# Optimization experiments

Measured on AMD Instinct MI355X. Metric: run time of the kernel, lower is better.

## Reference

```python
import jax, jax.numpy as jnp
import numpy as np

USER = 100000
ITEM = 200000
LATDIM = 128
GNN_LAYER = 3
UUGNN_LAYER = 2
N_EDGES = 600000
UU_EDGES = 300000


def setup_inputs() -> dict:
    key = jax.random.key(0)
    ks = jax.random.split(key, 8)
    N = USER + ITEM
    return {
        "uEmbeds0": jax.random.normal(ks[0], (USER, LATDIM), dtype=jnp.float32) * 0.05,
        "iEmbeds0": jax.random.normal(ks[1], (ITEM, LATDIM), dtype=jnp.float32) * 0.05,
        "adj_rows": jax.random.randint(ks[2], (N_EDGES,), 0, N, dtype=jnp.int32),
        "adj_cols": jax.random.randint(ks[3], (N_EDGES,), 0, N, dtype=jnp.int32),
        "adj_vals": jax.random.uniform(ks[4], (N_EDGES,), dtype=jnp.float32),
        "uadj_rows": jax.random.randint(ks[5], (UU_EDGES,), 0, USER, dtype=jnp.int32),
        "uadj_cols": jax.random.randint(ks[6], (UU_EDGES,), 0, USER, dtype=jnp.int32),
        "uadj_vals": jax.random.uniform(ks[7], (UU_EDGES,), dtype=jnp.float32),
    }


def _spmm(rows, cols, vals, x, n_rows):
    # out[r] = sum_{e: rows[e]==r} vals[e] * x[cols[e]]  (COO sparse @ dense)
    return jax.ops.segment_sum(vals[:, None] * x[cols], rows, num_segments=n_rows)


def reference(uEmbeds0, iEmbeds0, adj_rows, adj_cols, adj_vals,
              uadj_rows, uadj_cols, uadj_vals):
    N = USER + ITEM
    # LightGCN over bipartite adjacency, pool='sum' over layer-0..L embeddings
    # (dropout in eval mode -> identity)
    embeds = jnp.concatenate([uEmbeds0, iEmbeds0], axis=0)  # [N, d]
    acc = embeds
    for _ in range(GNN_LAYER):
        embeds = _spmm(adj_rows, adj_cols, adj_vals, embeds, N)
        acc = acc + embeds
    ui_uEmbed = acc[:USER]
    ui_iEmbed = acc[USER:]

    # LightGCN2 over user-user adjacency, sum of layer embeddings
    ulat = uEmbeds0
    uacc = ulat
    for _ in range(UUGNN_LAYER):
        ulat = _spmm(uadj_rows, uadj_cols, uadj_vals, ulat, USER)
        uacc = uacc + ulat
    return (ui_uEmbed, ui_iEmbed, uacc)
```

## Files before the change

### kernel.cpp

```cpp
#include <hip/hip_runtime.h>
#include <hip/hip_fp16.h>

#define USER_N   100000
#define ITEM_N   200000
#define LATDIM   128
#define NV4      32
#define N_TOTAL  300000
#define NR_ALL   400000
#define N_EDGES_C  600000
#define UU_EDGES_C 300000
#define NE_ALL   900000
#define SCAN_B   256

struct alignas(8) h4 { __half2 lo, hi; };

typedef float f4_ext __attribute__((ext_vector_type(4)));

__device__ __forceinline__ h4 to_h4(float4 a) {
    h4 r; r.lo = __floats2half2_rn(a.x, a.y); r.hi = __floats2half2_rn(a.z, a.w);
    return r;
}
__device__ __forceinline__ float4 to_f4(h4 h) {
    float2 l = __half22float2(h.lo), hh = __half22float2(h.hi);
    return make_float4(l.x, l.y, hh.x, hh.y);
}
__device__ __forceinline__ void fma4(float4& a, float v, float4 x) {
    a.x += v * x.x; a.y += v * x.y; a.z += v * x.z; a.w += v * x.w;
}
__device__ __forceinline__ float4 nt_load4(const float4* p) {
    f4_ext v = __builtin_nontemporal_load((const f4_ext*)p);
    return make_float4(v.x, v.y, v.z, v.w);
}
__device__ __forceinline__ void nt_store4(float4* p, float4 a) {
    f4_ext v = {a.x, a.y, a.z, a.w};
    __builtin_nontemporal_store(v, (f4_ext*)p);
}

__global__ void hist2_kernel(const int* __restrict__ ar, const int* __restrict__ ur,
                             int* __restrict__ cnt) {
    int i = blockIdx.x * blockDim.x + threadIdx.x;
    if (i < N_EDGES_C)      atomicAdd(&cnt[ar[i]], 1);
    else if (i < NE_ALL)    atomicAdd(&cnt[ur[i - N_EDGES_C] + N_TOTAL], 1);
}

__global__ void scan_block_kernel(const int* __restrict__ cnt,
                                  int* __restrict__ rptr,
                                  int* __restrict__ bsum, int n) {
    __shared__ int s[SCAN_B];
    int i = blockIdx.x * SCAN_B + threadIdx.x;
    int v = (i < n) ? cnt[i] : 0;
    s[threadIdx.x] = v;
    __syncthreads();
    for (int off = 1; off < SCAN_B; off <<= 1) {
        int t = (threadIdx.x >= off) ? s[threadIdx.x - off] : 0;
        __syncthreads();
        s[threadIdx.x] += t;
        __syncthreads();
    }
    if (i < n) rptr[i] = s[threadIdx.x] - v;
    if (threadIdx.x == SCAN_B - 1) bsum[blockIdx.x] = s[threadIdx.x];
}

__global__ void scan_bsum_kernel(int* __restrict__ bsum, int nb) {
    __shared__ int s[SCAN_B];
    __shared__ int carry;
    if (threadIdx.x == 0) carry = 0;
    __syncthreads();
    for (int base = 0; base < nb; base += SCAN_B) {
        int i = base + threadIdx.x;
        int v = (i < nb) ? bsum[i] : 0;
        s[threadIdx.x] = v;
        __syncthreads();
        for (int off = 1; off < SCAN_B; off <<= 1) {
            int t = (threadIdx.x >= off) ? s[threadIdx.x - off] : 0;
            __syncthreads();
            s[threadIdx.x] += t;
            __syncthreads();
        }
        if (i < nb) bsum[i] = s[threadIdx.x] - v + carry;
        __syncthreads();
        if (threadIdx.x == 0) carry += s[SCAN_B - 1];
        __syncthreads();
    }
}

__global__ void scan_add_kernel(int* __restrict__ rptr, const int* __restrict__ bsum,
                                int* __restrict__ cursor, int n, int n_edges) {
    int i = blockIdx.x * blockDim.x + threadIdx.x;
    if (i < n) {
        int v = rptr[i] + bsum[i / SCAN_B];
        rptr[i]   = v;
        cursor[i] = v;
    }
    if (i == 0) rptr[n] = n_edges;
}

__global__ void scatter2_kernel(const int* __restrict__ ar, const int* __restrict__ ac,
                                const float* __restrict__ av,
                                const int* __restrict__ ur, const int* __restrict__ uc,
                                const float* __restrict__ uv,
                                int* __restrict__ cursor,
                                int* __restrict__ scol, float* __restrict__ sval) {
    int i = blockIdx.x * blockDim.x + threadIdx.x;
    int r, c; float v;
    if (i < N_EDGES_C)      { r = ar[i];             c = ac[i];           v = av[i]; }
    else if (i < NE_ALL)    { int j = i - N_EDGES_C; r = ur[j] + N_TOTAL; c = uc[j] + N_TOTAL; v = uv[j]; }
    else return;
    int pos = atomicAdd(&cursor[r], 1);
    scol[pos] = c;
    sval[pos] = v;
}

__global__ void conv_kernel(const float4* __restrict__ uE,
                            const float4* __restrict__ iE,
                            h4* __restrict__ E16) {
    int i = blockIdx.x * blockDim.x + threadIdx.x;
    if (i >= N_TOTAL * NV4) return;
    const int ub = USER_N * NV4;
    float4 v = (i < ub) ? nt_load4(uE + i) : nt_load4(iE + (i - ub));
    E16[i] = to_h4(v);
}

__device__ __forceinline__ int e16_row(int c) {
    return (c < N_TOTAL) ? c : c - N_TOTAL;
}

__global__ void spmm_pass1(const int* __restrict__ rptr,
                           const int* __restrict__ scol,
                           const float* __restrict__ sval,
                           const h4* __restrict__ E16,
                           h4* __restrict__ cur1) {
    int t = blockIdx.x * blockDim.x + threadIdx.x;
    int r = t >> 5, sub = t & 31;
    if (r >= NR_ALL) return;
    int e0 = rptr[r], e1 = rptr[r + 1];

    float4 a0 = make_float4(0.f,0.f,0.f,0.f), a1 = a0;
    int e = e0;
    for (; e + 2 <= e1; e += 2) {
        int c0 = scol[e], c1 = scol[e + 1];
        float v0 = sval[e], v1 = sval[e + 1];
        h4 h0 = E16[(size_t)e16_row(c0) * NV4 + sub];
        h4 h1 = E16[(size_t)e16_row(c1) * NV4 + sub];
        fma4(a0, v0, to_f4(h0)); fma4(a1, v1, to_f4(h1));
    }
    if (e < e1) {
        int c0 = scol[e]; float v0 = sval[e];
        fma4(a0, v0, to_f4(E16[(size_t)e16_row(c0) * NV4 + sub]));
    }
    float4 a = make_float4(a0.x+a1.x, a0.y+a1.y, a0.z+a1.z, a0.w+a1.w);
    cur1[(size_t)r * NV4 + sub] = to_h4(a);
}

__global__ void spmm_pass2(const int* __restrict__ rptr,
                           const int* __restrict__ scol,
                           const float* __restrict__ sval,
                           const h4* __restrict__ cur1,
                           const h4* __restrict__ E16,
                           h4* __restrict__ cur2,
                           float4* __restrict__ uacc) {
    int t = blockIdx.x * blockDim.x + threadIdx.x;
    int r = t >> 5, sub = t & 31;
    if (r >= NR_ALL) return;
    int e0 = rptr[r], e1 = rptr[r + 1];

    float4 a0 = make_float4(0.f,0.f,0.f,0.f), a1 = a0;
    int e = e0;
    for (; e + 2 <= e1; e += 2) {
        int c0 = scol[e], c1 = scol[e + 1];
        float v0 = sval[e], v1 = sval[e + 1];
        h4 h0 = cur1[(size_t)c0 * NV4 + sub];
        h4 h1 = cur1[(size_t)c1 * NV4 + sub];
        fma4(a0, v0, to_f4(h0)); fma4(a1, v1, to_f4(h1));
    }
    if (e < e1) {
        int c0 = scol[e]; float v0 = sval[e];
        fma4(a0, v0, to_f4(cur1[(size_t)c0 * NV4 + sub]));
    }
    float4 a = make_float4(a0.x+a1.x, a0.y+a1.y, a0.z+a1.z, a0.w+a1.w);

    size_t o = (size_t)r * NV4 + sub;
    if (r < N_TOTAL) {
        cur2[o] = to_h4(a);
    } else {
        int ur = r - N_TOTAL;
        float4 u0 = to_f4(E16[(size_t)ur * NV4 + sub]);
        float4 l1 = to_f4(cur1[o]);
        nt_store4(uacc + (size_t)ur * NV4 + sub,
                  make_float4(u0.x + l1.x + a.x, u0.y + l1.y + a.y,
                              u0.z + l1.z + a.z, u0.w + l1.w + a.w));
    }
}

__global__ void spmm_pass3(const int* __restrict__ rptr,
                           const int* __restrict__ scol,
                           const float* __restrict__ sval,
                           const h4* __restrict__ cur2,
                           const h4* __restrict__ cur1,
                           const h4* __restrict__ E16,
                           float4* __restrict__ acc) {
    int t = blockIdx.x * blockDim.x + threadIdx.x;
    int r = t >> 5, sub = t & 31;
    if (r >= N_TOTAL) return;
    int e0 = rptr[r], e1 = rptr[r + 1];

    float4 a0 = make_float4(0.f,0.f,0.f,0.f), a1 = a0;
    int e = e0;
    for (; e + 2 <= e1; e += 2) {
        int c0 = scol[e], c1 = scol[e + 1];
        float v0 = sval[e], v1 = sval[e + 1];
        h4 h0 = cur2[(size_t)c0 * NV4 + sub];
        h4 h1 = cur2[(size_t)c1 * NV4 + sub];
        fma4(a0, v0, to_f4(h0)); fma4(a1, v1, to_f4(h1));
    }
    if (e < e1) {
        int c0 = scol[e]; float v0 = sval[e];
        fma4(a0, v0, to_f4(cur2[(size_t)c0 * NV4 + sub]));
    }
    float4 a = make_float4(a0.x+a1.x, a0.y+a1.y, a0.z+a1.z, a0.w+a1.w);

    size_t o = (size_t)r * NV4 + sub;
    float4 ez = to_f4(E16[o]);
    float4 l1 = to_f4(cur1[o]);
    float4 l2 = to_f4(cur2[o]);
    nt_store4(acc + o,
              make_float4(ez.x + l1.x + l2.x + a.x,
                          ez.y + l1.y + l2.y + a.y,
                          ez.z + l1.z + l2.z + a.z,
                          ez.w + l1.w + l2.w + a.w));
}

extern "C" void kernel_launch(void* const* d_in, const int* in_sizes, int n_in,
                              void* d_out, int out_size, void* d_ws, size_t ws_size,
                              hipStream_t stream) {
    const float* uE    = (const float*)d_in[0];
    const float* iE    = (const float*)d_in[1];
    const int*   arows = (const int*)  d_in[2];
    const int*   acols = (const int*)  d_in[3];
    const float* avals = (const float*)d_in[4];
    const int*   urows = (const int*)  d_in[5];
    const int*   ucols = (const int*)  d_in[6];
    const float* uvals = (const float*)d_in[7];

    float* acc  = (float*)d_out;
    float* uacc = acc + (size_t)N_TOTAL * LATDIM;

    h4*    E16  = (h4*)d_ws;
    h4*    cur1 = E16 + (size_t)N_TOTAL * NV4;
    h4*    cur2 = cur1 + (size_t)NR_ALL * NV4;
    int*   cnt  = (int*)(cur2 + (size_t)N_TOTAL * NV4);
    int*   rptr = cnt + NR_ALL;
    int*   curp = rptr + NR_ALL + 1;
    int*   bsum = curp + NR_ALL;
    int*   scol = bsum + 4096;
    float* sval = (float*)(scol + NE_ALL);

    const int TB = 256;

    hipMemsetAsync(cnt, 0, NR_ALL * sizeof(int), stream);
    hist2_kernel<<<(NE_ALL + TB - 1) / TB, TB, 0, stream>>>(arows, urows, cnt);
    {
        int nb = (NR_ALL + SCAN_B - 1) / SCAN_B;
        scan_block_kernel<<<nb, SCAN_B, 0, stream>>>(cnt, rptr, bsum, NR_ALL);
        scan_bsum_kernel<<<1, SCAN_B, 0, stream>>>(bsum, nb);
        scan_add_kernel<<<(NR_ALL + TB - 1) / TB, TB, 0, stream>>>(
            rptr, bsum, curp, NR_ALL, NE_ALL);
    }
    scatter2_kernel<<<(NE_ALL + TB - 1) / TB, TB, 0, stream>>>(
        arows, acols, avals, urows, ucols, uvals, curp, scol, sval);

    conv_kernel<<<(N_TOTAL * NV4 + TB - 1) / TB, TB, 0, stream>>>(
        (const float4*)uE, (const float4*)iE, E16);

    {
        int threads = NR_ALL * 32;
        int grid = (threads + TB - 1) / TB;
        spmm_pass1<<<grid, TB, 0, stream>>>(rptr, scol, sval, E16, cur1);
        spmm_pass2<<<grid, TB, 0, stream>>>(rptr, scol, sval, cur1, E16,
                                            cur2, (float4*)uacc);
    }
    {
        int threads = N_TOTAL * 32;
        int grid = (threads + TB - 1) / TB;
        spmm_pass3<<<grid, TB, 0, stream>>>(rptr, scol, sval, cur2, cur1, E16,
                                            (float4*)acc);
    }
}
```

Before: 382.0 us.

## Use 16-byte half8 rows, interleaved edge structs, and fuse conversion with histogram

The SpMM kernels now assign 16 threads per row, and each thread loads 16 bytes (8 halves) instead of 8, which halves the number of gather instructions per edge. Column index and value are stored together as one 8-byte Edge struct, so each edge needs one load instead of two. The fp16 conversion kernel is merged into the histogram kernel, removing one launch. Pass 3 also uses nontemporal loads for edges and residual terms. Wider per-thread work means fewer threads overall, which may expose less latency hiding on irregular gathers.

```diff
diff --git a/kernel.cpp b/kernel.cpp
--- a/kernel.cpp
+++ b/kernel.cpp
@@ -5,28 +5,25 @@
 #define ITEM_N   200000
 #define LATDIM   128
 #define NV4      32
+#define NV8      16
 #define N_TOTAL  300000
 #define NR_ALL   400000
 #define N_EDGES_C  600000
 #define UU_EDGES_C 300000
 #define NE_ALL   900000
 #define SCAN_B   256
-
-struct alignas(8) h4 { __half2 lo, hi; };
+#define CONV_T   (N_TOTAL * NV8)
+
+struct alignas(16) h8 { __half2 a, b, c, d; };
+struct alignas(8)  Edge { int c; float v; };
 
 typedef float f4_ext __attribute__((ext_vector_type(4)));
-
-__device__ __forceinline__ h4 to_h4(float4 a) {
-    h4 r; r.lo = __floats2half2_rn(a.x, a.y); r.hi = __floats2half2_rn(a.z, a.w);
-    return r;
-}
-__device__ __forceinline__ float4 to_f4(h4 h) {
-    float2 l = __half22float2(h.lo), hh = __half22float2(h.hi);
-    return make_float4(l.x, l.y, hh.x, hh.y);
-}
-__device__ __forceinline__ void fma4(float4& a, float v, float4 x) {
-    a.x += v * x.x; a.y += v * x.y; a.z += v * x.z; a.w += v * x.w;
-}
+typedef int   i4_ext __attribute__((ext_vector_type(4)));
+typedef int   i2_ext __attribute__((ext_vector_type(2)));
+
+union H8I { i4_ext i; h8 h; };
+union EDI { i2_ext i; Edge e; };
+
 __device__ __forceinline__ float4 nt_load4(const float4* p) {
     f4_ext v = __builtin_nontemporal_load((const f4_ext*)p);
     return make_float4(v.x, v.y, v.z, v.w);
@@ -35,12 +32,53 @@
     f4_ext v = {a.x, a.y, a.z, a.w};
     __builtin_nontemporal_store(v, (f4_ext*)p);
 }
-
-__global__ void hist2_kernel(const int* __restrict__ ar, const int* __restrict__ ur,
-                             int* __restrict__ cnt) {
-    int i = blockIdx.x * blockDim.x + threadIdx.x;
-    if (i < N_EDGES_C)      atomicAdd(&cnt[ar[i]], 1);
-    else if (i < NE_ALL)    atomicAdd(&cnt[ur[i - N_EDGES_C] + N_TOTAL], 1);
+__device__ __forceinline__ h8 nt_load_h8(const h8* p) {
+    H8I u; u.i = __builtin_nontemporal_load((const i4_ext*)p);
+    return u.h;
+}
+__device__ __forceinline__ Edge nt_load_edge(const Edge* p) {
+    EDI u; u.i = __builtin_nontemporal_load((const i2_ext*)p);
+    return u.e;
+}
+
+__device__ __forceinline__ h8 to_h8(float4 lo, float4 hi) {
+    h8 r;
+    r.a = __floats2half2_rn(lo.x, lo.y); r.b = __floats2half2_rn(lo.z, lo.w);
+    r.c = __floats2half2_rn(hi.x, hi.y); r.d = __floats2half2_rn(hi.z, hi.w);
+    return r;
+}
+__device__ __forceinline__ void h8_to_f(h8 h, float4& lo, float4& hi) {
+    float2 p = __half22float2(h.a), q = __half22float2(h.b);
+    float2 s = __half22float2(h.c), t = __half22float2(h.d);
+    lo = make_float4(p.x, p.y, q.x, q.y);
+    hi = make_float4(s.x, s.y, t.x, t.y);
+}
+__device__ __forceinline__ void fma4(float4& a, float v, float4 x) {
+    a.x += v * x.x; a.y += v * x.y; a.z += v * x.z; a.w += v * x.w;
+}
+__device__ __forceinline__ float4 add4(float4 a, float4 b) {
+    return make_float4(a.x + b.x, a.y + b.y, a.z + b.z, a.w + b.w);
+}
+
+__global__ void conv_hist_kernel(const float4* __restrict__ uE,
+                                 const float4* __restrict__ iE,
+                                 h8* __restrict__ E16,
+                                 const int* __restrict__ ar,
+                                 const int* __restrict__ ur,
+                                 int* __restrict__ cnt) {
+    int t = blockIdx.x * blockDim.x + threadIdx.x;
+    if (t < CONV_T) {
+        int f4i = t * 2;
+        const int ub = USER_N * NV4;
+        float4 lo, hi;
+        if (f4i < ub) { lo = nt_load4(uE + f4i);        hi = nt_load4(uE + f4i + 1); }
+        else          { lo = nt_load4(iE + (f4i - ub)); hi = nt_load4(iE + (f4i - ub) + 1); }
+        E16[t] = to_h8(lo, hi);
+    } else {
+        int i = t - CONV_T;
+        if (i < N_EDGES_C)   atomicAdd(&cnt[ar[i]], 1);
+        else if (i < NE_ALL) atomicAdd(&cnt[ur[i - N_EDGES_C] + N_TOTAL], 1);
+    }
 }
 
 __global__ void scan_block_kernel(const int* __restrict__ cnt,
@@ -100,25 +138,14 @@
                                 const int* __restrict__ ur, const int* __restrict__ uc,
                                 const float* __restrict__ uv,
                                 int* __restrict__ cursor,
-                                int* __restrict__ scol, float* __restrict__ sval) {
+                                Edge* __restrict__ edges) {
     int i = blockIdx.x * blockDim.x + threadIdx.x;
-    int r, c; float v;
-    if (i < N_EDGES_C)      { r = ar[i];             c = ac[i];           v = av[i]; }
-    else if (i < NE_ALL)    { int j = i - N_EDGES_C; r = ur[j] + N_TOTAL; c = uc[j] + N_TOTAL; v = uv[j]; }
+    int r; Edge ed;
+    if (i < N_EDGES_C)      { r = ar[i];             ed.c = ac[i];           ed.v = av[i]; }
+    else if (i < NE_ALL)    { int j = i - N_EDGES_C; r = ur[j] + N_TOTAL; ed.c = uc[j] + N_TOTAL; ed.v = uv[j]; }
     else return;
     int pos = atomicAdd(&cursor[r], 1);
-    scol[pos] = c;
-    sval[pos] = v;
-}
-
-__global__ void conv_kernel(const float4* __restrict__ uE,
-                            const float4* __restrict__ iE,
-                            h4* __restrict__ E16) {
-    int i = blockIdx.x * blockDim.x + threadIdx.x;
-    if (i >= N_TOTAL * NV4) return;
-    const int ub = USER_N * NV4;
-    float4 v = (i < ub) ? nt_load4(uE + i) : nt_load4(iE + (i - ub));
-    E16[i] = to_h4(v);
+    edges[pos] = ed;
 }
 
 __device__ __forceinline__ int e16_row(int c) {
@@ -126,108 +153,114 @@
 }
 
 __global__ void spmm_pass1(const int* __restrict__ rptr,
-                           const int* __restrict__ scol,
-                           const float* __restrict__ sval,
-                           const h4* __restrict__ E16,
-                           h4* __restrict__ cur1) {
+                           const Edge* __restrict__ edges,
+                           const h8* __restrict__ E16,
+                           h8* __restrict__ cur1) {
     int t = blockIdx.x * blockDim.x + threadIdx.x;
-    int r = t >> 5, sub = t & 31;
+    int r = t >> 4, sub = t & 15;
     if (r >= NR_ALL) return;
     int e0 = rptr[r], e1 = rptr[r + 1];
 
-    float4 a0 = make_float4(0.f,0.f,0.f,0.f), a1 = a0;
+    float4 a0l = make_float4(0,0,0,0), a0h = a0l, a1l = a0l, a1h = a0l;
     int e = e0;
     for (; e + 2 <= e1; e += 2) {
-        int c0 = scol[e], c1 = scol[e + 1];
-        float v0 = sval[e], v1 = sval[e + 1];
-        h4 h0 = E16[(size_t)e16_row(c0) * NV4 + sub];
-        h4 h1 = E16[(size_t)e16_row(c1) * NV4 + sub];
-        fma4(a0, v0, to_f4(h0)); fma4(a1, v1, to_f4(h1));
+        Edge d0 = edges[e], d1 = edges[e + 1];
+        h8 h0 = E16[(size_t)e16_row(d0.c) * NV8 + sub];
+        h8 h1 = E16[(size_t)e16_row(d1.c) * NV8 + sub];
+        float4 lo, hi;
+        h8_to_f(h0, lo, hi); fma4(a0l, d0.v, lo); fma4(a0h, d0.v, hi);
+        h8_to_f(h1, lo, hi); fma4(a1l, d1.v, lo); fma4(a1h, d1.v, hi);
     }
     if (e < e1) {
-        int c0 = scol[e]; float v0 = sval[e];
-        fma4(a0, v0, to_f4(E16[(size_t)e16_row(c0) * NV4 + sub]));
-    }
-    float4 a = make_float4(a0.x+a1.x, a0.y+a1.y, a0.z+a1.z, a0.w+a1.w);
-    cur1[(size_t)r * NV4 + sub] = to_h4(a);
+        Edge d0 = edges[e];
+        h8 h0 = E16[(size_t)e16_row(d0.c) * NV8 + sub];
+        float4 lo, hi;
+        h8_to_f(h0, lo, hi); fma4(a0l, d0.v, lo); fma4(a0h, d0.v, hi);
+    }
+    cur1[(size_t)r * NV8 + sub] = to_h8(add4(a0l, a1l), add4(a0h, a1h));
 }
 
 __global__ void spmm_pass2(const int* __restrict__ rptr,
-                           const int* __restrict__ scol,
-                           const float* __restrict__ sval,
-                           const h4* __restrict__ cur1,
-                           const h4* __restrict__ E16,
-                           h4* __restrict__ cur2,
+                           const Edge* __restrict__ edges,
+                           const h8* __restrict__ cur1,
+                           const h8* __restrict__ E16,
+                           h8* __restrict__ cur2,
                            float4* __restrict__ uacc) {
     int t = blockIdx.x * blockDim.x + threadIdx.x;
-    int r = t >> 5, sub = t & 31;
+    int r = t >> 4, sub = t & 15;
     if (r >= NR_ALL) return;
     int e0 = rptr[r], e1 = rptr[r + 1];
 
-    float4 a0 = make_float4(0.f,0.f,0.f,0.f), a1 = a0;
+    float4 a0l = make_float4(0,0,0,0), a0h = a0l, a1l = a0l, a1h = a0l;
     int e = e0;
     for (; e + 2 <= e1; e += 2) {
-        int c0 = scol[e], c1 = scol[e + 1];
-        float v0 = sval[e], v1 = sval[e + 1];
-        h4 h0 = cur1[(size_t)c0 * NV4 + sub];
-        h4 h1 = cur1[(size_t)c1 * NV4 + sub];
-        fma4(a0, v0, to_f4(h0)); fma4(a1, v1, to_f4(h1));
+        Edge d0 = edges[e], d1 = edges[e + 1];
+        h8 h0 = cur1[(size_t)d0.c * NV8 + sub];
+        h8 h1 = cur1[(size_t)d1.c * NV8 + sub];
+        float4 lo, hi;
+        h8_to_f(h0, lo, hi); fma4(a0l, d0.v, lo); fma4(a0h, d0.v, hi);
+        h8_to_f(h1, lo, hi); fma4(a1l, d1.v, lo); fma4(a1h, d1.v, hi);
     }
     if (e < e1) {
-        int c0 = scol[e]; float v0 = sval[e];
-        fma4(a0, v0, to_f4(cur1[(size_t)c0 * NV4 + sub]));
-    }
-    float4 a = make_float4(a0.x+a1.x, a0.y+a1.y, a0.z+a1.z, a0.w+a1.w);
-
-    size_t o = (size_t)r * NV4 + sub;
+        Edge d0 = edges[e];
+        h8 h0 = cur1[(size_t)d0.c * NV8 + sub];
+        float4 lo, hi;
+        h8_to_f(h0, lo, hi); fma4(a0l, d0.v, lo); fma4(a0h, d0.v, hi);
+    }
+    float4 al = add4(a0l, a1l), ah = add4(a0h, a1h);
+
+    size_t o = (size_t)r * NV8 + sub;
     if (r < N_TOTAL) {
-        cur2[o] = to_h4(a);
+        cur2[o] = to_h8(al, ah);
     } else {
         int ur = r - N_TOTAL;
-        float4 u0 = to_f4(E16[(size_t)ur * NV4 + sub]);
-        float4 l1 = to_f4(cur1[o]);
-        nt_store4(uacc + (size_t)ur * NV4 + sub,
-                  make_float4(u0.x + l1.x + a.x, u0.y + l1.y + a.y,
-                              u0.z + l1.z + a.z, u0.w + l1.w + a.w));
+        float4 u0l, u0h, l1l, l1h;
+        h8_to_f(E16[(size_t)ur * NV8 + sub], u0l, u0h);
+        h8_to_f(cur1[o], l1l, l1h);
+        size_t of4 = (size_t)ur * NV4 + sub * 2;
+        nt_store4(uacc + of4,     add4(add4(u0l, l1l), al));
+        nt_store4(uacc + of4 + 1, add4(add4(u0h, l1h), ah));
     }
 }
 
 __global__ void spmm_pass3(const int* __restrict__ rptr,
-                           const int* __restrict__ scol,
-                           const float* __restrict__ sval,
-                           const h4* __restrict__ cur2,
-                           const h4* __restrict__ cur1,
-                           const h4* __restrict__ E16,
+                           const Edge* __restrict__ edges,
+                           const h8* __restrict__ cur2,
+                           const h8* __restrict__ cur1,
+                           const h8* __restrict__ E16,
                            float4* __restrict__ acc) {
     int t = blockIdx.x * blockDim.x + threadIdx.x;
-    int r = t >> 5, sub = t & 31;
+    int r = t >> 4, sub = t & 15;
     if (r >= N_TOTAL) return;
     int e0 = rptr[r], e1 = rptr[r + 1];
 
-    float4 a0 = make_float4(0.f,0.f,0.f,0.f), a1 = a0;
+    float4 a0l = make_float4(0,0,0,0), a0h = a0l, a1l = a0l, a1h = a0l;
     int e = e0;
     for (; e + 2 <= e1; e += 2) {
-        int c0 = scol[e], c1 = scol[e + 1];
-        float v0 = sval[e], v1 = sval[e + 1];
-        h4 h0 = cur2[(size_t)c0 * NV4 + sub];
-        h4 h1 = cur2[(size_t)c1 * NV4 + sub];
-        fma4(a0, v0, to_f4(h0)); fma4(a1, v1, to_f4(h1));
+        Edge d0 = nt_load_edge(edges + e), d1 = nt_load_edge(edges + e + 1);
+        h8 h0 = cur2[(size_t)d0.c * NV8 + sub];
+        h8 h1 = cur2[(size_t)d1.c * NV8 + sub];
+        float4 lo, hi;
+        h8_to_f(h0, lo, hi); fma4(a0l, d0.v, lo); fma4(a0h, d0.v, hi);
+        h8_to_f(h1, lo, hi); fma4(a1l, d1.v, lo); fma4(a1h, d1.v, hi);
     }
     if (e < e1) {
-        int c0 = scol[e]; float v0 = sval[e];
-        fma4(a0, v0, to_f4(cur2[(size_t)c0 * NV4 + sub]));
-    }
-    float4 a = make_float4(a0.x+a1.x, a0.y+a1.y, a0.z+a1.z, a0.w+a1.w);
-
-    size_t o = (size_t)r * NV4 + sub;
-    float4 ez = to_f4(E16[o]);
-    float4 l1 = to_f4(cur1[o]);
-    float4 l2 = to_f4(cur2[o]);
-    nt_store4(acc + o,
-              make_float4(ez.x + l1.x + l2.x + a.x,
-                          ez.y + l1.y + l2.y + a.y,
-                          ez.z + l1.z + l2.z + a.z,
-                          ez.w + l1.w + l2.w + a.w));
+        Edge d0 = nt_load_edge(edges + e);
+        h8 h0 = cur2[(size_t)d0.c * NV8 + sub];
+        float4 lo, hi;
+        h8_to_f(h0, lo, hi); fma4(a0l, d0.v, lo); fma4(a0h, d0.v, hi);
+    }
+    float4 al = add4(a0l, a1l), ah = add4(a0h, a1h);
+
+    size_t o = (size_t)r * NV8 + sub;
+    float4 ezl, ezh, l1l, l1h, l2l, l2h;
+    h8_to_f(nt_load_h8(E16 + o),  ezl, ezh);
+    h8_to_f(nt_load_h8(cur1 + o), l1l, l1h);
+    h8_to_f(cur2[o], l2l, l2h);
+
+    size_t of4 = (size_t)r * NV4 + sub * 2;
+    nt_store4(acc + of4,     add4(add4(ezl, l1l), add4(l2l, al)));
+    nt_store4(acc + of4 + 1, add4(add4(ezh, l1h), add4(l2h, ah)));
 }
 
 extern "C" void kernel_launch(void* const* d_in, const int* in_sizes, int n_in,
@@ -245,20 +278,23 @@
     float* acc  = (float*)d_out;
     float* uacc = acc + (size_t)N_TOTAL * LATDIM;
 
-    h4*    E16  = (h4*)d_ws;
-    h4*    cur1 = E16 + (size_t)N_TOTAL * NV4;
-    h4*    cur2 = cur1 + (size_t)NR_ALL * NV4;
-    int*   cnt  = (int*)(cur2 + (size_t)N_TOTAL * NV4);
+    h8*    E16  = (h8*)d_ws;
+    h8*    cur1 = E16 + (size_t)N_TOTAL * NV8;
+    h8*    cur2 = cur1 + (size_t)NR_ALL * NV8;
+    int*   cnt  = (int*)(cur2 + (size_t)N_TOTAL * NV8);
     int*   rptr = cnt + NR_ALL;
     int*   curp = rptr + NR_ALL + 1;
     int*   bsum = curp + NR_ALL;
-    int*   scol = bsum + 4096;
-    float* sval = (float*)(scol + NE_ALL);
+    Edge*  edges = (Edge*)(bsum + 4096);
 
     const int TB = 256;
 
     hipMemsetAsync(cnt, 0, NR_ALL * sizeof(int), stream);
-    hist2_kernel<<<(NE_ALL + TB - 1) / TB, TB, 0, stream>>>(arows, urows, cnt);
+    {
+        int threads = CONV_T + NE_ALL;
+        conv_hist_kernel<<<(threads + TB - 1) / TB, TB, 0, stream>>>(
+            (const float4*)uE, (const float4*)iE, E16, arows, urows, cnt);
+    }
     {
         int nb = (NR_ALL + SCAN_B - 1) / SCAN_B;
         scan_block_kernel<<<nb, SCAN_B, 0, stream>>>(cnt, rptr, bsum, NR_ALL);
@@ -267,22 +303,19 @@
             rptr, bsum, curp, NR_ALL, NE_ALL);
     }
     scatter2_kernel<<<(NE_ALL + TB - 1) / TB, TB, 0, stream>>>(
-        arows, acols, avals, urows, ucols, uvals, curp, scol, sval);
-
-    conv_kernel<<<(N_TOTAL * NV4 + TB - 1) / TB, TB, 0, stream>>>(
-        (const float4*)uE, (const float4*)iE, E16);
+        arows, acols, avals, urows, ucols, uvals, curp, edges);
 
     {
-        int threads = NR_ALL * 32;
+        int threads = NR_ALL * NV8;
         int grid = (threads + TB - 1) / TB;
-        spmm_pass1<<<grid, TB, 0, stream>>>(rptr, scol, sval, E16, cur1);
-        spmm_pass2<<<grid, TB, 0, stream>>>(rptr, scol, sval, cur1, E16,
+        spmm_pass1<<<grid, TB, 0, stream>>>(rptr, edges, E16, cur1);
+        spmm_pass2<<<grid, TB, 0, stream>>>(rptr, edges, cur1, E16,
                                             cur2, (float4*)uacc);
     }
     {
-        int threads = N_TOTAL * 32;
+        int threads = N_TOTAL * NV8;
         int grid = (threads + TB - 1) / TB;
-        spmm_pass3<<<grid, TB, 0, stream>>>(rptr, scol, sval, cur2, cur1, E16,
+        spmm_pass3<<<grid, TB, 0, stream>>>(rptr, edges, cur2, cur1, E16,
                                             (float4*)acc);
     }
 }
```

After: 352.8 us. 7.6% less time.
